# Performance work log

Measured on AMD Instinct MI355X. Metric: run time of the kernel, lower is better.

The kernel has to match this reference:

```python
import jax, jax.numpy as jnp
import numpy as np

N = 50000      # nodes
E = 1600000    # edges (avg degree 32)
H = 2          # num_heads
F = 32         # att_feat
IN = 32        # in_feats (must equal att_feat, see w1(h_dst + g))
OUT = 32       # out_feats
NEG_SLOPE = 0.2


def setup_inputs() -> dict:
    key = jax.random.key(0)
    ks = jax.random.split(key, 11)
    s = 0.1  # param init scale
    return {
        "feat": jax.random.normal(ks[0], (N, IN), jnp.float32),
        "r_feat": jax.random.normal(ks[1], (E, H, F), jnp.float32),
        "src": jax.random.randint(ks[2], (E,), 0, N),
        "dst": jax.random.randint(ks[3], (E,), 0, N),
        "W1": jax.random.normal(ks[4], (IN, OUT), jnp.float32) * s,
        "b1": jnp.zeros((OUT,), jnp.float32),
        "W2s": jax.random.normal(ks[5], (IN, H * F), jnp.float32) * s,
        "b2s": jnp.zeros((H * F,), jnp.float32),
        "W2d": jax.random.normal(ks[6], (IN, H * F), jnp.float32) * s,
        "b2d": jnp.zeros((H * F,), jnp.float32),
        "attn": jax.random.normal(ks[7], (1, H, F), jnp.float32) * s,
    }


def reference(feat, r_feat, src, dst, W1, b1, W2s, b2s, W2d, b2d, attn):
    n = feat.shape[0]
    # projections (dropout = 0 -> identity)
    feat_src = (feat @ W2s + b2s).reshape(n, H, F)   # [N,H,F]
    feat_dst = (feat @ W2d + b2d).reshape(n, H, F)   # [N,H,F]
    en = feat_src[src]                                # [E,H,F] gather
    ev = feat_dst[dst]                                # [E,H,F] gather
    # u_add_v + leaky_relu, dot with attention vector
    e = jax.nn.leaky_relu(en + ev, negative_slope=NEG_SLOPE)
    e = jnp.sum(e * attn, axis=-1, keepdims=True)     # [E,H,1]
    # edge_softmax: softmax over incoming edges of each dst node
    m = jax.ops.segment_max(e, dst, num_segments=n)   # [N,H,1]
    m = jnp.where(jnp.isfinite(m), m, 0.0)            # zero in-degree -> -inf
    ee = jnp.exp(e - m[dst])                          # [E,H,1]
    denom = jax.ops.segment_sum(ee, dst, num_segments=n)
    alpha = ee / jnp.maximum(denom[dst], 1e-9)        # [E,H,1]
    # message: softmax over feature dim of (en * rr * alpha)
    msg = jax.nn.softmax(en * r_feat * alpha, axis=-1)  # [E,H,F]
    g_agg = jax.ops.segment_sum(msg, dst, num_segments=n)  # [N,H,F]
    g_sum = jnp.sum(g_agg, axis=1)                    # att_agg='sum' -> [N,F]
    rst = (feat + g_sum) @ W1 + b1                    # [N,OUT]
    return rst
```

## Files before the change

kernel.cpp:

```cpp
#include <hip/hip_runtime.h>

#define N_NODES 50000
#define E_EDGES 1600000
#define NHEAD 2
#define FDIM 32
#define HF 64
#define IN_F 32
#define OUT_F 32
#define CAPB 128

__device__ __forceinline__ int rl(int v, int l) { return __builtin_amdgcn_readlane(v, l); }

template<int CTRL>
__device__ __forceinline__ float dpp_add(float v) {
    int t = __builtin_amdgcn_update_dpp(0, __float_as_int(v), CTRL, 0xf, 0xf, true);
    return v + __int_as_float(t);
}
__device__ __forceinline__ float red4_sum(float v) {
    v = dpp_add<0xB1>(v);
    v = dpp_add<0x4E>(v);
    return v;
}
template<int PAT>
__device__ __forceinline__ float swz_add(float v) {
    return v + __int_as_float(__builtin_amdgcn_ds_swizzle(__float_as_int(v), PAT));
}
__device__ __forceinline__ float red64_sum(float v) {
    v = red4_sum(v);
    v = swz_add<0x101F>(v);
    v = swz_add<0x201F>(v);
    v = swz_add<0x401F>(v);
    v += __shfl_xor(v, 32, 64);
    return v;
}
__device__ __forceinline__ void load8(float* d, const float* __restrict__ p) {
    *(float4*)&d[0] = *(const float4*)&p[0];
    *(float4*)&d[4] = *(const float4*)&p[4];
}

__global__ void proj_kernel(const float* __restrict__ feat,
                            const float* __restrict__ W2s, const float* __restrict__ b2s,
                            const float* __restrict__ W2d, const float* __restrict__ b2d,
                            float* __restrict__ fsrc, float* __restrict__ fdst,
                            int* __restrict__ cur) {
    int idx = blockIdx.x * blockDim.x + threadIdx.x;
    int n = idx >> 6;
    int c = idx & 63;
    if (n >= N_NODES) return;
    if (c == 0) cur[n] = 0;
    const float* frow = feat + n * IN_F;
    float s = b2s[c];
    float d = b2d[c];
    #pragma unroll
    for (int k = 0; k < IN_F; ++k) {
        float fv = frow[k];
        s += fv * W2s[k * HF + c];
        d += fv * W2d[k * HF + c];
    }
    fsrc[n * HF + c] = s;
    fdst[n * HF + c] = d;
}

__global__ void scatter_kernel(const int4* __restrict__ src4, const int4* __restrict__ dst4,
                               int* __restrict__ cur, int2* __restrict__ pairs) {
    int i = blockIdx.x * blockDim.x + threadIdx.x;
    if (i * 4 < E_EDGES) {
        int4 s = src4[i];
        int4 d = dst4[i];
        int e = 4 * i;
        int p0 = atomicAdd(&cur[d.x], 1);
        if (p0 < CAPB) pairs[(size_t)d.x * CAPB + p0] = make_int2(s.x, e + 0);
        int p1 = atomicAdd(&cur[d.y], 1);
        if (p1 < CAPB) pairs[(size_t)d.y * CAPB + p1] = make_int2(s.y, e + 1);
        int p2 = atomicAdd(&cur[d.z], 1);
        if (p2 < CAPB) pairs[(size_t)d.z * CAPB + p2] = make_int2(s.z, e + 2);
        int p3 = atomicAdd(&cur[d.w], 1);
        if (p3 < CAPB) pairs[(size_t)d.w * CAPB + p3] = make_int2(s.w, e + 3);
    }
}

__global__ __launch_bounds__(256) void agg_kernel(
        const int* __restrict__ cur, const int2* __restrict__ pairs,
        const float* __restrict__ fsrc, const float* __restrict__ fdst,
        const float* __restrict__ rfeat, const float* __restrict__ attn,
        const float* __restrict__ feat,
        const float* __restrict__ W1, const float* __restrict__ b1,
        float* __restrict__ out) {
    __shared__ int2  pairsL[4][CAPB];
    __shared__ float eeL[4][CAPB];
    __shared__ __align__(16) float gpart[2][NHEAD][FDIM];
    int tid = threadIdx.x;
    int wib = tid >> 6;
    int nb = wib >> 1;
    int h = wib & 1;
    int n = blockIdx.x * 2 + nb;
    int lane = tid & 63;
    int eL = lane >> 2;
    int q = lane & 3;
    int deg = min(cur[n], CAPB);
    const int2* bucket = pairs + (size_t)n * CAPB;

    pairsL[wib][lane]      = (lane < deg)      ? bucket[lane]      : make_int2(0, 0);
    pairsL[wib][64 + lane] = (64 + lane < deg) ? bucket[64 + lane] : make_int2(0, 0);

    int hq = h * FDIM + q * 8;
    float ev[8], aw[8];
    load8(ev, fdst + n * HF + hq);
    load8(aw, attn + hq);

    int nst = (deg + 15) >> 4;

    float denp = 0.0f;
    for (int j = 0; j < nst; ++j) {
        int idx = j * 16 + eL;
        int2 se = pairsL[wib][idx];
        float en[8];
        load8(en, fsrc + se.x * HF + hq);
        float acc = 0.0f;
        #pragma unroll
        for (int k = 0; k < 8; ++k) {
            float x = en[k] + ev[k];
            x = fmaxf(x, 0.2f * x);
            acc = fmaf(x, aw[k], acc);
        }
        float v = red4_sum(acc);
        float E = __expf(v);
        if (q == 0) eeL[wib][idx] = E;
        denp += (idx < deg) ? E : 0.0f;
    }
    float den = red64_sum(denp) * 0.25f;
    float dinv = __builtin_amdgcn_rcpf(fmaxf(den, 1e-9f));

    float g[8] = {0, 0, 0, 0, 0, 0, 0, 0};
    for (int j = 0; j < nst; ++j) {
        int idx = j * 16 + eL;
        int2 se = pairsL[wib][idx];
        bool valid = idx < deg;
        float a = valid ? eeL[wib][idx] * dinv : 0.0f;
        float en[8], r[8], p[8];
        load8(en, fsrc + se.x * HF + hq);
        load8(r, rfeat + (size_t)se.y * HF + hq);
        float S = 0.0f;
        #pragma unroll
        for (int k = 0; k < 8; ++k) {
            p[k] = __expf(en[k] * r[k] * a);
            S += p[k];
        }
        S = red4_sum(S);
        float w = valid ? __builtin_amdgcn_rcpf(S) : 0.0f;
        #pragma unroll
        for (int k = 0; k < 8; ++k) g[k] = fmaf(p[k], w, g[k]);
    }

    #pragma unroll
    for (int k = 0; k < 8; ++k) {
        float v = g[k];
        v = swz_add<0x101F>(v);
        v = swz_add<0x201F>(v);
        v = swz_add<0x401F>(v);
        v += __shfl_xor(v, 32, 64);
        g[k] = v;
    }
    if (lane < 4) {
        *(float4*)&gpart[nb][h][lane * 8]     = make_float4(g[0], g[1], g[2], g[3]);
        *(float4*)&gpart[nb][h][lane * 8 + 4] = make_float4(g[4], g[5], g[6], g[7]);
    }
    __syncthreads();

    if (h == 0) {
        int f = lane & 31;
        float gs = gpart[nb][0][f] + gpart[nb][1][f];
        float x = feat[n * IN_F + f] + gs;
        float acc = b1[f];
        #pragma unroll
        for (int k = 0; k < 32; ++k) {
            float xk = __int_as_float(rl(__float_as_int(x), k));
            acc = fmaf(xk, W1[k * OUT_F + f], acc);
        }
        if (lane < 32) out[n * OUT_F + f] = acc;
    }
}

extern "C" void kernel_launch(void* const* d_in, const int* in_sizes, int n_in,
                              void* d_out, int out_size, void* d_ws, size_t ws_size,
                              hipStream_t stream) {
    const float* feat  = (const float*)d_in[0];
    const float* rfeat = (const float*)d_in[1];
    const int*   src   = (const int*)d_in[2];
    const int*   dst   = (const int*)d_in[3];
    const float* W1    = (const float*)d_in[4];
    const float* b1    = (const float*)d_in[5];
    const float* W2s   = (const float*)d_in[6];
    const float* b2s   = (const float*)d_in[7];
    const float* W2d   = (const float*)d_in[8];
    const float* b2d   = (const float*)d_in[9];
    const float* attn  = (const float*)d_in[10];
    float* out = (float*)d_out;

    float* fsrc = (float*)d_ws;
    float* fdst = fsrc + (size_t)N_NODES * HF;
    int*   cur  = (int*)(fdst + (size_t)N_NODES * HF);
    int2*  pairs = (int2*)(cur + N_NODES);

    const int BLK = 256;
    proj_kernel<<<(N_NODES * HF + BLK - 1) / BLK, BLK, 0, stream>>>(
        feat, W2s, b2s, W2d, b2d, fsrc, fdst, cur);
    scatter_kernel<<<(E_EDGES / 4 + BLK - 1) / BLK, BLK, 0, stream>>>(
        (const int4*)src, (const int4*)dst, cur, pairs);
    agg_kernel<<<N_NODES / 2, BLK, 0, stream>>>(
        cur, pairs, fsrc, fdst, rfeat, attn, feat, W1, b1, out);
}
```

Baseline: 275.9 us.

## Keep gathered edge features in registers via degree-specialized unrolled aggregation

Replaces the LDS staging of edge pairs and exp scores with a templated body, specialized by 16-edge step count (up to 4 steps, deg<=64), that loads all source-feature gathers up front into registers. Each edge's fsrc row is then gathered once instead of twice, and the loads can all be in flight together. The rfeat load overlaps the score computation. Nodes above 64 degree fall back to a loop that re-reads pairs from global memory and recomputes scores. Register pressure rises with NST=4 and may lower occupancy.

```diff
diff --git a/kernel.cpp b/kernel.cpp
--- a/kernel.cpp
+++ b/kernel.cpp
@@ -79,6 +79,56 @@
     }
 }
 
+template<int NST>
+__device__ __forceinline__ void agg_body(
+        int deg, const int2* __restrict__ bucket,
+        const float* __restrict__ fsrc, const float* __restrict__ rfeat,
+        const float ev[8], const float aw[8], int hq, int eL, float g[8]) {
+    int2 se[NST];
+    float en[NST][8];
+    #pragma unroll
+    for (int j = 0; j < NST; ++j) {
+        int idx = j * 16 + eL;
+        se[j] = make_int2(0, 0);
+        if (idx < deg) se[j] = bucket[idx];
+        load8(en[j], fsrc + se[j].x * HF + hq);
+    }
+    float E[NST];
+    float denp = 0.0f;
+    #pragma unroll
+    for (int j = 0; j < NST; ++j) {
+        float acc = 0.0f;
+        #pragma unroll
+        for (int k = 0; k < 8; ++k) {
+            float x = en[j][k] + ev[k];
+            x = fmaxf(x, 0.2f * x);
+            acc = fmaf(x, aw[k], acc);
+        }
+        float v = red4_sum(acc);
+        E[j] = (j * 16 + eL < deg) ? __expf(v) : 0.0f;
+        denp += E[j];
+    }
+    float den = red64_sum(denp) * 0.25f;
+    float dinv = __builtin_amdgcn_rcpf(fmaxf(den, 1e-9f));
+    #pragma unroll
+    for (int j = 0; j < NST; ++j) {
+        float r[8];
+        load8(r, rfeat + (size_t)se[j].y * HF + hq);
+        float a = E[j] * dinv;
+        float p[8];
+        float S = 0.0f;
+        #pragma unroll
+        for (int k = 0; k < 8; ++k) {
+            p[k] = __expf(en[j][k] * r[k] * a);
+            S += p[k];
+        }
+        S = red4_sum(S);
+        float w = (j * 16 + eL < deg) ? __builtin_amdgcn_rcpf(S) : 0.0f;
+        #pragma unroll
+        for (int k = 0; k < 8; ++k) g[k] = fmaf(p[k], w, g[k]);
+    }
+}
+
 __global__ __launch_bounds__(256) void agg_kernel(
         const int* __restrict__ cur, const int2* __restrict__ pairs,
         const float* __restrict__ fsrc, const float* __restrict__ fdst,
@@ -86,8 +136,6 @@
         const float* __restrict__ feat,
         const float* __restrict__ W1, const float* __restrict__ b1,
         float* __restrict__ out) {
-    __shared__ int2  pairsL[4][CAPB];
-    __shared__ float eeL[4][CAPB];
     __shared__ __align__(16) float gpart[2][NHEAD][FDIM];
     int tid = threadIdx.x;
     int wib = tid >> 6;
@@ -100,56 +148,66 @@
     int deg = min(cur[n], CAPB);
     const int2* bucket = pairs + (size_t)n * CAPB;
 
-    pairsL[wib][lane]      = (lane < deg)      ? bucket[lane]      : make_int2(0, 0);
-    pairsL[wib][64 + lane] = (64 + lane < deg) ? bucket[64 + lane] : make_int2(0, 0);
-
     int hq = h * FDIM + q * 8;
     float ev[8], aw[8];
     load8(ev, fdst + n * HF + hq);
     load8(aw, attn + hq);
 
-    int nst = (deg + 15) >> 4;
-
-    float denp = 0.0f;
-    for (int j = 0; j < nst; ++j) {
-        int idx = j * 16 + eL;
-        int2 se = pairsL[wib][idx];
-        float en[8];
-        load8(en, fsrc + se.x * HF + hq);
-        float acc = 0.0f;
-        #pragma unroll
-        for (int k = 0; k < 8; ++k) {
-            float x = en[k] + ev[k];
-            x = fmaxf(x, 0.2f * x);
-            acc = fmaf(x, aw[k], acc);
-        }
-        float v = red4_sum(acc);
-        float E = __expf(v);
-        if (q == 0) eeL[wib][idx] = E;
-        denp += (idx < deg) ? E : 0.0f;
-    }
-    float den = red64_sum(denp) * 0.25f;
-    float dinv = __builtin_amdgcn_rcpf(fmaxf(den, 1e-9f));
-
     float g[8] = {0, 0, 0, 0, 0, 0, 0, 0};
-    for (int j = 0; j < nst; ++j) {
-        int idx = j * 16 + eL;
-        int2 se = pairsL[wib][idx];
-        bool valid = idx < deg;
-        float a = valid ? eeL[wib][idx] * dinv : 0.0f;
-        float en[8], r[8], p[8];
-        load8(en, fsrc + se.x * HF + hq);
-        load8(r, rfeat + (size_t)se.y * HF + hq);
-        float S = 0.0f;
-        #pragma unroll
-        for (int k = 0; k < 8; ++k) {
-            p[k] = __expf(en[k] * r[k] * a);
-            S += p[k];
-        }
-        S = red4_sum(S);
-        float w = valid ? __builtin_amdgcn_rcpf(S) : 0.0f;
-        #pragma unroll
-        for (int k = 0; k < 8; ++k) g[k] = fmaf(p[k], w, g[k]);
+    if (deg <= 64) {
+        int nst = (deg + 15) >> 4;
+        if (nst <= 1)      agg_body<1>(deg, bucket, fsrc, rfeat, ev, aw, hq, eL, g);
+        else if (nst == 2) agg_body<2>(deg, bucket, fsrc, rfeat, ev, aw, hq, eL, g);
+        else if (nst == 3) agg_body<3>(deg, bucket, fsrc, rfeat, ev, aw, hq, eL, g);
+        else               agg_body<4>(deg, bucket, fsrc, rfeat, ev, aw, hq, eL, g);
+    } else {
+        int nst = (deg + 15) >> 4;
+        float denp = 0.0f;
+        for (int j = 0; j < nst; ++j) {
+            int idx = j * 16 + eL;
+            int2 se = make_int2(0, 0);
+            if (idx < deg) se = pairs[(size_t)n * CAPB + idx];
+            float en[8];
+            load8(en, fsrc + se.x * HF + hq);
+            float acc = 0.0f;
+            #pragma unroll
+            for (int k = 0; k < 8; ++k) {
+                float x = en[k] + ev[k];
+                x = fmaxf(x, 0.2f * x);
+                acc = fmaf(x, aw[k], acc);
+            }
+            float v = red4_sum(acc);
+            denp += (idx < deg) ? __expf(v) : 0.0f;
+        }
+        float den = red64_sum(denp) * 0.25f;
+        float dinv = __builtin_amdgcn_rcpf(fmaxf(den, 1e-9f));
+        for (int j = 0; j < nst; ++j) {
+            int idx = j * 16 + eL;
+            int2 se = make_int2(0, 0);
+            if (idx < deg) se = pairs[(size_t)n * CAPB + idx];
+            float en[8], r[8], p[8];
+            load8(en, fsrc + se.x * HF + hq);
+            load8(r, rfeat + (size_t)se.y * HF + hq);
+            float acc = 0.0f;
+            #pragma unroll
+            for (int k = 0; k < 8; ++k) {
+                float x = en[k] + ev[k];
+                x = fmaxf(x, 0.2f * x);
+                acc = fmaf(x, aw[k], acc);
+            }
+            float v = red4_sum(acc);
+            float a = ((idx < deg) ? __expf(v) : 0.0f) * dinv;
+            float S = 0.0f;
+            #pragma unroll
+            for (int k = 0; k < 8; ++k) {
+                p[k] = __expf(en[k] * r[k] * a);
+                S += p[k];
+            }
+            S = red4_sum(S);
+            float w = (idx < deg) ? __builtin_amdgcn_rcpf(S) : 0.0f;
+            #pragma unroll
+            for (int k = 0; k < 8; ++k) g[k] = fmaf(p[k], w, g[k]);
+        }
     }
 
     #pragma unroll
```

New measurement: 272.9 us. No clear change (-1.1%).
